# Kernel tuning notes

Hardware: AMD Instinct MI355X
Metric: run time of the kernel (lower is better)

The kernel has to match this reference:

```python
import jax, jax.numpy as jnp
import numpy as np

B, F, L, P, H = 32, 64, 8192, 96, 8
HD = F // H
EPS_ATTN = 1e-6
EPS_REVIN = 1e-5
EPS_LN = 1e-5


def setup_inputs() -> dict:
    key = jax.random.key(0)
    ks = jax.random.split(key, 8)
    f32 = jnp.float32
    return {
        'x': jax.random.normal(ks[0], (B, F, L), dtype=f32),
        'gamma': jnp.ones((1, 1, F), dtype=f32),
        'beta': jnp.zeros((1, 1, F), dtype=f32),
        'ln_w': jnp.ones((F,), dtype=f32),
        'ln_b': jnp.zeros((F,), dtype=f32),
        'Wq': 0.05 * jax.random.normal(ks[1], (F, F), dtype=f32),
        'bq': jnp.zeros((F,), dtype=f32),
        'Wk': 0.05 * jax.random.normal(ks[2], (F, F), dtype=f32),
        'bk': jnp.zeros((F,), dtype=f32),
        'Wv': 0.05 * jax.random.normal(ks[3], (F, F), dtype=f32),
        'bv': jnp.zeros((F,), dtype=f32),
        'Wo': 0.05 * jax.random.normal(ks[4], (F, F), dtype=f32),
        'bo': jnp.zeros((F,), dtype=f32),
        'Wlin': 0.01 * jax.random.normal(ks[5], (P, L), dtype=f32),
        'blin': jnp.zeros((P,), dtype=f32),
        'Wp': 0.1 * jax.random.normal(ks[6], (1, F), dtype=f32),
        'bp': jnp.zeros((1,), dtype=f32),
    }


def _phi(t):
    # feature map: elu(x) + 1 (non-negative)
    return jax.nn.elu(t) + 1.0


def _layernorm(h, w, b):
    mu = jnp.mean(h, axis=-1, keepdims=True)
    var = jnp.mean(jnp.square(h - mu), axis=-1, keepdims=True)
    return (h - mu) * jax.lax.rsqrt(var + EPS_LN) * w + b


def reference(x, gamma, beta, ln_w, ln_b, Wq, bq, Wk, bk, Wv, bv, Wo, bo,
              Wlin, blin, Wp, bp):
    # (B, F, L) -> (B, L, F)
    xt = jnp.transpose(x, (0, 2, 1))
    # RevIN norm (stats over time axis, detached; torch std is unbiased ddof=1)
    mean = jax.lax.stop_gradient(jnp.mean(xt, axis=1, keepdims=True))
    std = jax.lax.stop_gradient(jnp.std(xt, axis=1, keepdims=True, ddof=1) + EPS_REVIN)
    xn = (xt - mean) / std * gamma + beta
    residual = xn
    h = _layernorm(xn, ln_w, ln_b)
    # Q/K/V projections (torch Linear: h @ W.T + b)
    Q = h @ Wq.T + bq
    K = h @ Wk.T + bk
    V = h @ Wv.T + bv
    # (B, L, F) -> (B, H, L, HD)
    def heads(t):
        return jnp.transpose(t.reshape(B, L, H, HD), (0, 2, 1, 3))
    Q, K, V = heads(Q), heads(K), heads(V)
    Q, K = _phi(Q), _phi(K)
    # linear attention: phi(Q) (phi(K)^T V) / (phi(Q) sum_n phi(K))
    KV = jnp.einsum('bhnd,bhne->bhde', K, V)           # (B,H,HD,HD)
    out = jnp.einsum('bhnd,bhde->bhne', Q, KV)          # (B,H,L,HD)
    Z = jnp.sum(K, axis=2)                              # (B,H,HD)
    normalizer = jnp.einsum('bhnd,bhd->bhn', Q, Z)[..., None] + EPS_ATTN
    out = out / normalizer
    out = jnp.transpose(out, (0, 2, 1, 3)).reshape(B, L, F)
    out = out @ Wo.T + bo
    y = out + residual                                  # (B, L, F)
    # temporal linear: (B, F, L) @ Wlin.T -> (B, F, P) -> (B, P, F)
    y = jnp.transpose(jnp.transpose(y, (0, 2, 1)) @ Wlin.T + blin, (0, 2, 1))
    # RevIN denorm
    y = (y - beta) / gamma
    y = y * std + mean
    # projector to scalar per step
    return (y @ Wp.T + bp)[..., 0]                      # (B, P)
```

## Files before the change

kernel.cpp:

```cpp
#include <hip/hip_runtime.h>
#include <cstddef>

#define NB 32
#define NF 64
#define NL 8192
#define NP 96
#define NH 8
#define TSPLIT 32

#define WS_MEAN 0
#define WS_STD  2048
#define WS_RSTD 4096
#define WS_KV   6144
#define WS_Z    22528
#define WS_OUT2 24576
#define WS_WLB  221184
#define WS_YT   614400

typedef __bf16 bfx8 __attribute__((ext_vector_type(8)));
typedef float f32x4 __attribute__((ext_vector_type(4)));
#define MFMA16(a, b, c) __builtin_amdgcn_mfma_f32_16x16x32_bf16((a), (b), (c), 0, 0, 0)

__device__ __forceinline__ unsigned short f2bf(float f) {
  unsigned u = __float_as_uint(f);
  unsigned r = u + 0x7FFFu + ((u >> 16) & 1u);
  return (unsigned short)(r >> 16);
}
__device__ __forceinline__ unsigned packbf2(float lo, float hi) {
  return (unsigned)f2bf(lo) | ((unsigned)f2bf(hi) << 16);
}
__device__ __forceinline__ float bflo(unsigned d) { return __uint_as_float(d << 16); }
__device__ __forceinline__ float bfhi(unsigned d) { return __uint_as_float(d & 0xFFFF0000u); }
__device__ __forceinline__ float bf1(unsigned short s) { return __uint_as_float(((unsigned)s) << 16); }

__device__ __forceinline__ bfx8 ldfrag(const unsigned short* p) {
  uint4 u = *(const uint4*)p;
  return __builtin_bit_cast(bfx8, u);
}

__global__ __launch_bounds__(256) void k_stats(const float* __restrict__ x,
                                               float* __restrict__ wmean,
                                               float* __restrict__ wstd,
                                               float* __restrict__ wrstd) {
  int bf = blockIdx.x;
  int tid = threadIdx.x;
  const float4* row4 = (const float4*)(x + (size_t)bf * NL);
  float s1 = 0.f, s2 = 0.f;
#pragma unroll
  for (int i = 0; i < NL / 4 / 256; i++) {
    float4 v = row4[tid + i * 256];
    s1 += v.x + v.y + v.z + v.w;
    s2 += v.x * v.x + v.y * v.y + v.z * v.z + v.w * v.w;
  }
  __shared__ float r1[256], r2[256];
  r1[tid] = s1; r2[tid] = s2;
  __syncthreads();
  for (int off = 128; off > 0; off >>= 1) {
    if (tid < off) { r1[tid] += r1[tid + off]; r2[tid] += r2[tid + off]; }
    __syncthreads();
  }
  if (tid == 0) {
    float m = r1[0] * (1.f / NL);
    float var = (r2[0] - (float)NL * m * m) * (1.f / (NL - 1));
    float sd = sqrtf(fmaxf(var, 0.f)) + 1e-5f;
    wmean[bf] = m;
    wstd[bf] = sd;
    wrstd[bf] = 1.f / sd;
  }
}

__global__ __launch_bounds__(256) void k_wlb(const float* __restrict__ Wlin,
                                             unsigned short* __restrict__ wlb) {
  int i = blockIdx.x * 256 + threadIdx.x;
  float4 v = ((const float4*)Wlin)[i];
  uint2 o; o.x = packbf2(v.x, v.y); o.y = packbf2(v.z, v.w);
  *(uint2*)&wlb[i * 4] = o;
}

__global__ __launch_bounds__(256, 4) void k_kv(
    const float* __restrict__ x,
    const float* __restrict__ gamma, const float* __restrict__ beta,
    const float* __restrict__ lnw, const float* __restrict__ lnb,
    const float* __restrict__ Wk, const float* __restrict__ bk,
    const float* __restrict__ Wv, const float* __restrict__ bv,
    const float* __restrict__ wmean, const float* __restrict__ wrstd,
    float* __restrict__ wKV, float* __restrict__ wZ) {
  __shared__ __align__(16) char smem[40960];
  unsigned short* hA  = (unsigned short*)smem;
  unsigned short* WkB = (unsigned short*)(smem + 18432);
  unsigned short* WvB = (unsigned short*)(smem + 27648);
  unsigned short* pK  = (unsigned short*)smem;
  unsigned short* pV  = (unsigned short*)(smem + 17408);
  float* SkT   = (float*)(smem + 36864);
  float* Tpart = (float*)(smem + 37888);
  float* mun   = (float*)(smem + 39936);
  float* rsn   = (float*)(smem + 40448);

  const int tid = threadIdx.x;
  const int b = blockIdx.x >> 6;
  const int L0 = (blockIdx.x & 63) * 128;
  const int lane = tid & 63, wv = tid >> 6;
  const int mm = lane & 15, qd = lane >> 4;

  {
    int jj = tid >> 2, g = tid & 3;
    int f0 = g * 16;
    float tkp = 0.f, tvp = 0.f;
#pragma unroll
    for (int i = 0; i < 4; i++) {
      int f = f0 + i * 4;
      float4 wk4 = *(const float4*)&Wk[jj * NF + f];
      float4 wv4 = *(const float4*)&Wv[jj * NF + f];
      float4 lw  = *(const float4*)&lnw[f];
      float4 lb  = *(const float4*)&lnb[f];
      uint2 pk2, pv2;
      pk2.x = packbf2(wk4.x * lw.x, wk4.y * lw.y);
      pk2.y = packbf2(wk4.z * lw.z, wk4.w * lw.w);
      pv2.x = packbf2(wv4.x * lw.x, wv4.y * lw.y);
      pv2.y = packbf2(wv4.z * lw.z, wv4.w * lw.w);
      *(uint2*)&WkB[jj * 72 + f] = pk2;
      *(uint2*)&WvB[jj * 72 + f] = pv2;
      tkp += lb.x * wk4.x + lb.y * wk4.y + lb.z * wk4.z + lb.w * wk4.w;
      tvp += lb.x * wv4.x + lb.y * wv4.y + lb.z * wv4.z + lb.w * wv4.w;
    }
    Tpart[g * 64 + jj] = tkp;
    Tpart[256 + g * 64 + jj] = tvp;
  }

  if (tid < 128) {
    float xn[NF];
    float mu = 0.f;
#pragma unroll
    for (int f = 0; f < NF; f++) {
      float v = x[((size_t)(b * NF + f)) * NL + L0 + tid];
      v = (v - wmean[b * NF + f]) * wrstd[b * NF + f] * gamma[f] + beta[f];
      xn[f] = v; mu += v;
    }
    mu *= (1.f / NF);
    float var = 0.f;
#pragma unroll
    for (int f = 0; f < NF; f++) { float d = xn[f] - mu; var += d * d; }
    float rs = rsqrtf(var * (1.f / NF) + 1e-5f);
    mun[tid] = mu; rsn[tid] = rs;
    unsigned* hrow = (unsigned*)&hA[tid * 72];
#pragma unroll
    for (int f2 = 0; f2 < 32; f2++)
      hrow[f2] = packbf2(xn[2 * f2], xn[2 * f2 + 1]);
  }
  __syncthreads();

  if (tid < 128) {
    int sel = tid >> 6, j = tid & 63;
    const unsigned* wr = (const unsigned*)((sel ? WvB : WkB) + j * 72);
    float s = 0.f;
#pragma unroll
    for (int i = 0; i < 32; i++) { unsigned d = wr[i]; s += bflo(d) + bfhi(d); }
    float t = Tpart[sel * 256 + j] + Tpart[sel * 256 + 64 + j] +
              Tpart[sel * 256 + 128 + j] + Tpart[sel * 256 + 192 + j];
    t += sel ? bv[j] : bk[j];
    SkT[sel * 128 + j] = s;
    SkT[sel * 128 + 64 + j] = t;
  }
  __syncthreads();

  const f32x4 fz = {0.f, 0.f, 0.f, 0.f};
  f32x4 kacc[2][4], vacc[2][4];
#pragma unroll
  for (int i = 0; i < 2; i++)
#pragma unroll
    for (int jt = 0; jt < 4; jt++) { kacc[i][jt] = fz; vacc[i][jt] = fz; }

#pragma unroll
  for (int kc = 0; kc < 2; kc++) {
    bfx8 a0 = ldfrag(&hA[(wv * 32 + mm) * 72 + kc * 32 + qd * 8]);
    bfx8 a1 = ldfrag(&hA[(wv * 32 + 16 + mm) * 72 + kc * 32 + qd * 8]);
#pragma unroll
    for (int jt = 0; jt < 4; jt++) {
      bfx8 bkf = ldfrag(&WkB[(jt * 16 + mm) * 72 + kc * 32 + qd * 8]);
      bfx8 bvf = ldfrag(&WvB[(jt * 16 + mm) * 72 + kc * 32 + qd * 8]);
      kacc[0][jt] = MFMA16(a0, bkf, kacc[0][jt]);
      kacc[1][jt] = MFMA16(a1, bkf, kacc[1][jt]);
      vacc[0][jt] = MFMA16(a0, bvf, vacc[0][jt]);
      vacc[1][jt] = MFMA16(a1, bvf, vacc[1][jt]);
    }
  }

#pragma unroll
  for (int lt2 = 0; lt2 < 2; lt2++) {
    float4 mu4 = *(const float4*)&mun[wv * 32 + lt2 * 16 + qd * 4];
    float4 rs4 = *(const float4*)&rsn[wv * 32 + lt2 * 16 + qd * 4];
    float muv[4] = {mu4.x, mu4.y, mu4.z, mu4.w};
    float rsv[4] = {rs4.x, rs4.y, rs4.z, rs4.w};
#pragma unroll
    for (int jt = 0; jt < 4; jt++) {
      int j = jt * 16 + mm;
      float Sk = SkT[j], Tk = SkT[64 + j], Sv = SkT[128 + j], Tv = SkT[192 + j];
#pragma unroll
      for (int r = 0; r < 4; r++) {
        float kk = rsv[r] * (kacc[lt2][jt][r] - muv[r] * Sk) + Tk;
        kacc[lt2][jt][r] = (kk > 0.f) ? (kk + 1.f) : __expf(kk);
        vacc[lt2][jt][r] = rsv[r] * (vacc[lt2][jt][r] - muv[r] * Sv) + Tv;
      }
    }
  }
  __syncthreads();

#pragma unroll
  for (int lt2 = 0; lt2 < 2; lt2++) {
    int l0 = wv * 32 + lt2 * 16 + qd * 4;
#pragma unroll
    for (int jt = 0; jt < 4; jt++) {
      int j = jt * 16 + mm;
      uint2 dk, dv;
      dk.x = packbf2(kacc[lt2][jt][0], kacc[lt2][jt][1]);
      dk.y = packbf2(kacc[lt2][jt][2], kacc[lt2][jt][3]);
      dv.x = packbf2(vacc[lt2][jt][0], vacc[lt2][jt][1]);
      dv.y = packbf2(vacc[lt2][jt][2], vacc[lt2][jt][3]);
      *(uint2*)&pK[j * 136 + l0] = dk;
      *(uint2*)&pV[j * 136 + l0] = dv;
    }
  }
  __syncthreads();

  {
    f32x4 racc = fz;
#pragma unroll
    for (int kb = 0; kb < 4; kb++) {
      bfx8 ak = ldfrag(&pK[(wv * 16 + mm) * 136 + kb * 32 + qd * 8]);
      bfx8 bv8 = ldfrag(&pV[(wv * 16 + mm) * 136 + kb * 32 + qd * 8]);
      racc = MFMA16(ak, bv8, racc);
    }
    int eh = mm >> 3, e = mm & 7;
#pragma unroll
    for (int r = 0; r < 4; r++) {
      int row = qd * 4 + r;
      if ((row >> 3) == eh)
        atomicAdd(&wKV[(b * NH + wv * 2 + eh) * 64 + (row & 7) * 8 + e], racc[r]);
    }
  }
  if (tid < 64) {
    const unsigned* kr = (const unsigned*)&pK[tid * 136];
    float zs = 0.f;
#pragma unroll
    for (int i = 0; i < 64; i++) { unsigned d = kr[i]; zs += bflo(d) + bfhi(d); }
    atomicAdd(&wZ[b * 64 + tid], zs);
  }
}

__global__ __launch_bounds__(256, 2) void k_qy(
    const float* __restrict__ x,
    const float* __restrict__ gamma, const float* __restrict__ beta,
    const float* __restrict__ lnw, const float* __restrict__ lnb,
    const float* __restrict__ Wq, const float* __restrict__ bq,
    const float* __restrict__ Wo, const float* __restrict__ bo,
    const float* __restrict__ wmean, const float* __restrict__ wrstd,
    const float* __restrict__ wKV, const float* __restrict__ wZ,
    unsigned short* __restrict__ yTb) {
  __shared__ __align__(16) char smem[60160];
  unsigned short* hA  = (unsigned short*)smem;
  unsigned short* WqB = (unsigned short*)(smem + 18432);
  unsigned short* WoB = (unsigned short*)(smem + 27648);
  unsigned short* qaA = (unsigned short*)(smem + 36864);
  float* kvz   = (float*)(smem + 55296);
  float* mun   = (float*)(smem + 57600);
  float* rsn   = (float*)(smem + 58112);
  float* SqTq  = (float*)(smem + 58624);
  float* Tpart = (float*)(smem + 59136);

  const int tid = threadIdx.x;
  const int b = blockIdx.x >> 6;
  const int L0 = (blockIdx.x & 63) * 128;
  const int lane = tid & 63, wv = tid >> 6;
  const int mm = lane & 15, qd = lane >> 4;

  {
    int jj = tid >> 2, g = tid & 3;
    int f0 = g * 16;
    float tqp = 0.f;
#pragma unroll
    for (int i = 0; i < 4; i++) {
      int f = f0 + i * 4;
      float4 wq4 = *(const float4*)&Wq[jj * NF + f];
      float4 wo4 = *(const float4*)&Wo[jj * NF + f];
      float4 lw  = *(const float4*)&lnw[f];
      float4 lb  = *(const float4*)&lnb[f];
      uint2 pq2, po2;
      pq2.x = packbf2(wq4.x * lw.x, wq4.y * lw.y);
      pq2.y = packbf2(wq4.z * lw.z, wq4.w * lw.w);
      po2.x = packbf2(wo4.x, wo4.y);
      po2.y = packbf2(wo4.z, wo4.w);
      *(uint2*)&WqB[jj * 72 + f] = pq2;
      *(uint2*)&WoB[jj * 72 + f] = po2;
      tqp += lb.x * wq4.x + lb.y * wq4.y + lb.z * wq4.z + lb.w * wq4.w;
    }
    Tpart[g * 64 + jj] = tqp;
  }
  for (int i = tid; i < 576; i += 256)
    kvz[i] = (i < 512) ? wKV[b * 512 + i] : wZ[b * 64 + i - 512];

  if (tid < 128) {
    float xn[NF];
    float mu = 0.f;
#pragma unroll
    for (int f = 0; f < NF; f++) {
      float v = x[((size_t)(b * NF + f)) * NL + L0 + tid];
      v = (v - wmean[b * NF + f]) * wrstd[b * NF + f] * gamma[f] + beta[f];
      xn[f] = v; mu += v;
    }
    mu *= (1.f / NF);
    float var = 0.f;
#pragma unroll
    for (int f = 0; f < NF; f++) { float d = xn[f] - mu; var += d * d; }
    float rs = rsqrtf(var * (1.f / NF) + 1e-5f);
    mun[tid] = mu; rsn[tid] = rs;
    unsigned* hrow = (unsigned*)&hA[tid * 72];
#pragma unroll
    for (int f2 = 0; f2 < 32; f2++)
      hrow[f2] = packbf2(xn[2 * f2], xn[2 * f2 + 1]);
  }
  __syncthreads();

  if (tid < 64) {
    const unsigned* wr = (const unsigned*)(WqB + tid * 72);
    float s = 0.f;
#pragma unroll
    for (int i = 0; i < 32; i++) { unsigned d = wr[i]; s += bflo(d) + bfhi(d); }
    float t = Tpart[tid] + Tpart[64 + tid] + Tpart[128 + tid] + Tpart[192 + tid] + bq[tid];
    SqTq[tid] = s; SqTq[64 + tid] = t;
  }
  __syncthreads();

  const f32x4 fz = {0.f, 0.f, 0.f, 0.f};

  {
    f32x4 qacc[2][4];
#pragma unroll
    for (int i = 0; i < 2; i++)
#pragma unroll
      for (int jt = 0; jt < 4; jt++) qacc[i][jt] = fz;
#pragma unroll
    for (int kc = 0; kc < 2; kc++) {
      bfx8 a0 = ldfrag(&hA[(wv * 32 + mm) * 72 + kc * 32 + qd * 8]);
      bfx8 a1 = ldfrag(&hA[(wv * 32 + 16 + mm) * 72 + kc * 32 + qd * 8]);
#pragma unroll
      for (int jt = 0; jt < 4; jt++) {
        bfx8 bqf = ldfrag(&WqB[(jt * 16 + mm) * 72 + kc * 32 + qd * 8]);
        qacc[0][jt] = MFMA16(a0, bqf, qacc[0][jt]);
        qacc[1][jt] = MFMA16(a1, bqf, qacc[1][jt]);
      }
    }
#pragma unroll
    for (int lt2 = 0; lt2 < 2; lt2++) {
      float4 mu4 = *(const float4*)&mun[wv * 32 + lt2 * 16 + qd * 4];
      float4 rs4 = *(const float4*)&rsn[wv * 32 + lt2 * 16 + qd * 4];
      float muv[4] = {mu4.x, mu4.y, mu4.z, mu4.w};
      float rsv[4] = {rs4.x, rs4.y, rs4.z, rs4.w};
      int l0 = wv * 32 + lt2 * 16 + qd * 4;
#pragma unroll
      for (int jt = 0; jt < 4; jt++) {
        int j = jt * 16 + mm;
        float Sj = SqTq[j], Tj = SqTq[64 + j];
#pragma unroll
        for (int r = 0; r < 4; r++) {
          float q = rsv[r] * (qacc[lt2][jt][r] - muv[r] * Sj) + Tj;
          q = (q > 0.f) ? (q + 1.f) : __expf(q);
          qaA[(l0 + r) * 72 + j] = f2bf(q);
        }
      }
    }
  }
  __syncthreads();

  {
    int lt = tid & 31, hd = tid >> 5;
    int lbase = lt * 4;
    float qv[4][8];
#pragma unroll
    for (int i = 0; i < 4; i++) {
      uint4 u = *(const uint4*)&qaA[(lbase + i) * 72 + hd * 8];
      qv[i][0] = bflo(u.x); qv[i][1] = bfhi(u.x);
      qv[i][2] = bflo(u.y); qv[i][3] = bfhi(u.y);
      qv[i][4] = bflo(u.z); qv[i][5] = bfhi(u.z);
      qv[i][6] = bflo(u.w); qv[i][7] = bfhi(u.w);
    }
    float att[4][8], nrm[4];
#pragma unroll
    for (int i = 0; i < 4; i++) {
      nrm[i] = 1e-6f;
#pragma unroll
      for (int e = 0; e < 8; e++) att[i][e] = 0.f;
    }
#pragma unroll
    for (int d = 0; d < 8; d++) {
      float zd = kvz[512 + hd * 8 + d];
      float4 kva = *(const float4*)&kvz[hd * 64 + d * 8];
      float4 kvb = *(const float4*)&kvz[hd * 64 + d * 8 + 4];
#pragma unroll
      for (int i = 0; i < 4; i++) {
        float qq = qv[i][d];
        nrm[i] = fmaf(qq, zd, nrm[i]);
        att[i][0] = fmaf(qq, kva.x, att[i][0]);
        att[i][1] = fmaf(qq, kva.y, att[i][1]);
        att[i][2] = fmaf(qq, kva.z, att[i][2]);
        att[i][3] = fmaf(qq, kva.w, att[i][3]);
        att[i][4] = fmaf(qq, kvb.x, att[i][4]);
        att[i][5] = fmaf(qq, kvb.y, att[i][5]);
        att[i][6] = fmaf(qq, kvb.z, att[i][6]);
        att[i][7] = fmaf(qq, kvb.w, att[i][7]);
      }
    }
#pragma unroll
    for (int i = 0; i < 4; i++) {
      float inv = 1.f / nrm[i];
      uint4 o;
      o.x = packbf2(att[i][0] * inv, att[i][1] * inv);
      o.y = packbf2(att[i][2] * inv, att[i][3] * inv);
      o.z = packbf2(att[i][4] * inv, att[i][5] * inv);
      o.w = packbf2(att[i][6] * inv, att[i][7] * inv);
      *(uint4*)&qaA[(lbase + i) * 72 + hd * 8] = o;
    }
  }
  __syncthreads();

  {
    f32x4 yacc[2][4];
#pragma unroll
    for (int i = 0; i < 2; i++)
#pragma unroll
      for (int ft = 0; ft < 4; ft++) yacc[i][ft] = fz;
#pragma unroll
    for (int ec = 0; ec < 2; ec++) {
      bfx8 a0 = ldfrag(&qaA[(wv * 32 + mm) * 72 + ec * 32 + qd * 8]);
      bfx8 a1 = ldfrag(&qaA[(wv * 32 + 16 + mm) * 72 + ec * 32 + qd * 8]);
#pragma unroll
      for (int ft = 0; ft < 4; ft++) {
        bfx8 bof = ldfrag(&WoB[(ft * 16 + mm) * 72 + ec * 32 + qd * 8]);
        yacc[0][ft] = MFMA16(a0, bof, yacc[0][ft]);
        yacc[1][ft] = MFMA16(a1, bof, yacc[1][ft]);
      }
    }
#pragma unroll
    for (int lt2 = 0; lt2 < 2; lt2++) {
      int l0 = wv * 32 + lt2 * 16 + qd * 4;
#pragma unroll
      for (int ft = 0; ft < 4; ft++) {
        int ff = ft * 16 + mm;
        float bof = bo[ff];
        float v0 = yacc[lt2][ft][0] + bf1(hA[(l0 + 0) * 72 + ff]) + bof;
        float v1 = yacc[lt2][ft][1] + bf1(hA[(l0 + 1) * 72 + ff]) + bof;
        float v2 = yacc[lt2][ft][2] + bf1(hA[(l0 + 2) * 72 + ff]) + bof;
        float v3 = yacc[lt2][ft][3] + bf1(hA[(l0 + 3) * 72 + ff]) + bof;
        uint2 o2;
        o2.x = packbf2(v0, v1);
        o2.y = packbf2(v2, v3);
        *(uint2*)&yTb[((size_t)(b * NF + ff)) * NL + L0 + l0] = o2;
      }
    }
  }
}

__global__ __launch_bounds__(256) void k_temporal(
    const unsigned short* __restrict__ yTb, const unsigned short* __restrict__ wlb,
    float* __restrict__ out2) {
  const int tid = threadIdx.x, lane = tid & 63, wvx = tid >> 6;
  const int mm = lane & 15, qd = lane >> 4;
  const int b = blockIdx.x / TSPLIT;
  const int kc = blockIdx.x % TSPLIT;
  const int Lc = NL / TSPLIT;
  const unsigned short* yrow = yTb + ((size_t)(b * NF + wvx * 16 + mm)) * NL + kc * Lc + qd * 8;
  const unsigned short* wrow = wlb + (size_t)mm * NL + kc * Lc + qd * 8;
  const f32x4 fz = {0.f, 0.f, 0.f, 0.f};
  f32x4 acc[6];
#pragma unroll
  for (int pt = 0; pt < 6; pt++) acc[pt] = fz;

#pragma unroll 2
  for (int ks = 0; ks < Lc / 32; ks++) {
    bfx8 bfr = ldfrag(yrow + ks * 32);
#pragma unroll
    for (int pt = 0; pt < 6; pt++) {
      bfx8 afr = ldfrag(wrow + (size_t)(pt * 16) * NL + ks * 32);
      acc[pt] = MFMA16(afr, bfr, acc[pt]);
    }
  }
  const int ff = wvx * 16 + mm;
#pragma unroll
  for (int pt = 0; pt < 6; pt++) {
#pragma unroll
    for (int r = 0; r < 4; r++) {
      int p = pt * 16 + qd * 4 + r;
      atomicAdd(&out2[((size_t)(b * NP + p)) * NF + ff], acc[pt][r]);
    }
  }
}

__global__ __launch_bounds__(64) void k_final(
    const float* __restrict__ out2, const float* __restrict__ blin,
    const float* __restrict__ gamma, const float* __restrict__ beta,
    const float* __restrict__ wmean, const float* __restrict__ wstd,
    const float* __restrict__ Wp, const float* __restrict__ bp,
    float* __restrict__ out) {
  int b = blockIdx.x / NP;
  int p = blockIdx.x % NP;
  int f = threadIdx.x;
  float v = out2[((size_t)(b * NP + p)) * NF + f] + blin[p];
  v = (v - beta[f]) / gamma[f];
  v = v * wstd[b * NF + f] + wmean[b * NF + f];
  float s = v * Wp[f];
#pragma unroll
  for (int off = 32; off > 0; off >>= 1)
    s += __shfl_down(s, off, 64);
  if (f == 0) out[blockIdx.x] = s + bp[0];
}

extern "C" void kernel_launch(void* const* d_in, const int* in_sizes, int n_in,
                              void* d_out, int out_size, void* d_ws, size_t ws_size,
                              hipStream_t stream) {
  const float* x     = (const float*)d_in[0];
  const float* gamma = (const float*)d_in[1];
  const float* beta  = (const float*)d_in[2];
  const float* lnw   = (const float*)d_in[3];
  const float* lnb   = (const float*)d_in[4];
  const float* Wq    = (const float*)d_in[5];
  const float* bq    = (const float*)d_in[6];
  const float* Wk    = (const float*)d_in[7];
  const float* bk    = (const float*)d_in[8];
  const float* Wv    = (const float*)d_in[9];
  const float* bv    = (const float*)d_in[10];
  const float* Wo    = (const float*)d_in[11];
  const float* bo    = (const float*)d_in[12];
  const float* Wlin  = (const float*)d_in[13];
  const float* blin  = (const float*)d_in[14];
  const float* Wp    = (const float*)d_in[15];
  const float* bp    = (const float*)d_in[16];
  float* out = (float*)d_out;
  float* ws  = (float*)d_ws;

  float* wmean = ws + WS_MEAN;
  float* wstd  = ws + WS_STD;
  float* wrstd = ws + WS_RSTD;
  float* wKV   = ws + WS_KV;
  float* wZ    = ws + WS_Z;
  float* wout2 = ws + WS_OUT2;
  unsigned short* wlb = (unsigned short*)(ws + WS_WLB);
  unsigned short* yTb = (unsigned short*)(ws + WS_YT);

  (void)hipMemsetAsync(wKV, 0, (size_t)(16384 + 2048 + 196608) * sizeof(float), stream);

  k_stats<<<NB * NF, 256, 0, stream>>>(x, wmean, wstd, wrstd);
  k_wlb<<<NP * NL / 4 / 256, 256, 0, stream>>>(Wlin, wlb);
  k_kv<<<NB * 64, 256, 0, stream>>>(x, gamma, beta, lnw, lnb, Wk, bk, Wv, bv,
                                    wmean, wrstd, wKV, wZ);
  k_qy<<<NB * 64, 256, 0, stream>>>(x, gamma, beta, lnw, lnb, Wq, bq, Wo, bo,
                                    wmean, wrstd, wKV, wZ, yTb);
  k_temporal<<<NB * TSPLIT, 256, 0, stream>>>(yTb, wlb, wout2);
  k_final<<<NB * NP, 64, 0, stream>>>(wout2, blin, gamma, beta, wmean, wstd, Wp, bp, out);
}
```

Baseline: 247.1 us.

## Cache normalized bf16 activations from k_kv and retile yT/Wlin for contiguous MFMA loads

k_kv now writes its bf16 normalized tile and per-row LayerNorm stats to workspace, so k_qy no longer rereads fp32 x and redoes RevIN/LayerNorm. k_qy drops to a smaller LDS footprint, which lets it raise occupancy to 3 blocks per CU, and it reads the residual from the global bf16 tile. The yT and Wlin bf16 buffers are re-laid out in 32-wide L blocks so k_temporal's fragment loads are contiguous. The cost is extra global writes and reads (a 16 MB bf16 intermediate) and a larger workspace.

```diff
diff --git a/kernel.cpp b/kernel.cpp
--- a/kernel.cpp
+++ b/kernel.cpp
@@ -14,8 +14,11 @@
 #define WS_KV   6144
 #define WS_Z    22528
 #define WS_OUT2 24576
-#define WS_WLB  221184
-#define WS_YT   614400
+#define WS_MUN  221184
+#define WS_RSN  483328
+#define WS_WLB  745472
+#define WS_XNB  1138688
+#define WS_YT   9527296
 
 typedef __bf16 bfx8 __attribute__((ext_vector_type(8)));
 typedef float f32x4 __attribute__((ext_vector_type(4)));
@@ -72,9 +75,14 @@
 __global__ __launch_bounds__(256) void k_wlb(const float* __restrict__ Wlin,
                                              unsigned short* __restrict__ wlb) {
   int i = blockIdx.x * 256 + threadIdx.x;
-  float4 v = ((const float4*)Wlin)[i];
-  uint2 o; o.x = packbf2(v.x, v.y); o.y = packbf2(v.z, v.w);
-  *(uint2*)&wlb[i * 4] = o;
+  int p = i >> 10;
+  int l8 = (i & 1023) * 8;
+  float4 va = *(const float4*)&Wlin[(size_t)p * NL + l8];
+  float4 vb = *(const float4*)&Wlin[(size_t)p * NL + l8 + 4];
+  uint4 o;
+  o.x = packbf2(va.x, va.y); o.y = packbf2(va.z, va.w);
+  o.z = packbf2(vb.x, vb.y); o.w = packbf2(vb.z, vb.w);
+  *(uint4*)&wlb[(((size_t)(l8 >> 5)) * NP + p) * 32 + (l8 & 31)] = o;
 }
 
 __global__ __launch_bounds__(256, 4) void k_kv(
@@ -84,7 +92,9 @@
     const float* __restrict__ Wk, const float* __restrict__ bk,
     const float* __restrict__ Wv, const float* __restrict__ bv,
     const float* __restrict__ wmean, const float* __restrict__ wrstd,
-    float* __restrict__ wKV, float* __restrict__ wZ) {
+    float* __restrict__ wKV, float* __restrict__ wZ,
+    float* __restrict__ wmun, float* __restrict__ wrsn,
+    unsigned short* __restrict__ xnb) {
   __shared__ __align__(16) char smem[40960];
   unsigned short* hA  = (unsigned short*)smem;
   unsigned short* WkB = (unsigned short*)(smem + 18432);
@@ -98,7 +108,8 @@
 
   const int tid = threadIdx.x;
   const int b = blockIdx.x >> 6;
-  const int L0 = (blockIdx.x & 63) * 128;
+  const int tI = blockIdx.x & 63;
+  const int L0 = tI * 128;
   const int lane = tid & 63, wv = tid >> 6;
   const int mm = lane & 15, qd = lane >> 4;
 
@@ -142,12 +153,21 @@
     for (int f = 0; f < NF; f++) { float d = xn[f] - mu; var += d * d; }
     float rs = rsqrtf(var * (1.f / NF) + 1e-5f);
     mun[tid] = mu; rsn[tid] = rs;
+    wmun[(size_t)b * NL + L0 + tid] = mu;
+    wrsn[(size_t)b * NL + L0 + tid] = rs;
     unsigned* hrow = (unsigned*)&hA[tid * 72];
 #pragma unroll
     for (int f2 = 0; f2 < 32; f2++)
       hrow[f2] = packbf2(xn[2 * f2], xn[2 * f2 + 1]);
   }
   __syncthreads();
+
+  {
+    int row = tid >> 1, half = tid & 1;
+    const uint4* s4 = (const uint4*)&hA[row * 72 + half * 32];
+    uint4* d4 = (uint4*)(xnb + (((size_t)(b * 64 + tI) * 128 + row) * 64 + half * 32));
+    d4[0] = s4[0]; d4[1] = s4[1]; d4[2] = s4[2]; d4[3] = s4[3];
+  }
 
   if (tid < 128) {
     int sel = tid >> 6, j = tid & 63;
@@ -247,31 +267,32 @@
   }
 }
 
-__global__ __launch_bounds__(256, 2) void k_qy(
-    const float* __restrict__ x,
-    const float* __restrict__ gamma, const float* __restrict__ beta,
+__global__ __launch_bounds__(256, 3) void k_qy(
+    const unsigned short* __restrict__ xnb,
     const float* __restrict__ lnw, const float* __restrict__ lnb,
     const float* __restrict__ Wq, const float* __restrict__ bq,
     const float* __restrict__ Wo, const float* __restrict__ bo,
-    const float* __restrict__ wmean, const float* __restrict__ wrstd,
+    const float* __restrict__ wmun, const float* __restrict__ wrsn,
     const float* __restrict__ wKV, const float* __restrict__ wZ,
-    unsigned short* __restrict__ yTb) {
-  __shared__ __align__(16) char smem[60160];
+    unsigned short* __restrict__ ytb) {
+  __shared__ __align__(16) char smem[41728];
   unsigned short* hA  = (unsigned short*)smem;
+  unsigned short* qaA = (unsigned short*)smem;
   unsigned short* WqB = (unsigned short*)(smem + 18432);
   unsigned short* WoB = (unsigned short*)(smem + 27648);
-  unsigned short* qaA = (unsigned short*)(smem + 36864);
-  float* kvz   = (float*)(smem + 55296);
-  float* mun   = (float*)(smem + 57600);
-  float* rsn   = (float*)(smem + 58112);
-  float* SqTq  = (float*)(smem + 58624);
-  float* Tpart = (float*)(smem + 59136);
+  float* kvz   = (float*)(smem + 36864);
+  float* mun   = (float*)(smem + 39168);
+  float* rsn   = (float*)(smem + 39680);
+  float* SqTq  = (float*)(smem + 40192);
+  float* Tpart = (float*)(smem + 40704);
 
   const int tid = threadIdx.x;
   const int b = blockIdx.x >> 6;
-  const int L0 = (blockIdx.x & 63) * 128;
+  const int tI = blockIdx.x & 63;
+  const int L0 = tI * 128;
   const int lane = tid & 63, wv = tid >> 6;
   const int mm = lane & 15, qd = lane >> 4;
+  const unsigned short* xtile = xnb + (size_t)(b * 64 + tI) * 128 * 64;
 
   {
     int jj = tid >> 2, g = tid & 3;
@@ -297,26 +318,16 @@
   }
   for (int i = tid; i < 576; i += 256)
     kvz[i] = (i < 512) ? wKV[b * 512 + i] : wZ[b * 64 + i - 512];
-
+  {
+    int row = tid >> 1, half = tid & 1;
+    const uint4* s4 = (const uint4*)(xtile + (size_t)row * 64 + half * 32);
+    uint4 u0 = s4[0], u1 = s4[1], u2 = s4[2], u3 = s4[3];
+    uint4* d4 = (uint4*)&hA[row * 72 + half * 32];
+    d4[0] = u0; d4[1] = u1; d4[2] = u2; d4[3] = u3;
+  }
   if (tid < 128) {
-    float xn[NF];
-    float mu = 0.f;
-#pragma unroll
-    for (int f = 0; f < NF; f++) {
-      float v = x[((size_t)(b * NF + f)) * NL + L0 + tid];
-      v = (v - wmean[b * NF + f]) * wrstd[b * NF + f] * gamma[f] + beta[f];
-      xn[f] = v; mu += v;
-    }
-    mu *= (1.f / NF);
-    float var = 0.f;
-#pragma unroll
-    for (int f = 0; f < NF; f++) { float d = xn[f] - mu; var += d * d; }
-    float rs = rsqrtf(var * (1.f / NF) + 1e-5f);
-    mun[tid] = mu; rsn[tid] = rs;
-    unsigned* hrow = (unsigned*)&hA[tid * 72];
-#pragma unroll
-    for (int f2 = 0; f2 < 32; f2++)
-      hrow[f2] = packbf2(xn[2 * f2], xn[2 * f2 + 1]);
+    mun[tid] = wmun[(size_t)b * NL + L0 + tid];
+    rsn[tid] = wrsn[(size_t)b * NL + L0 + tid];
   }
   __syncthreads();
 
@@ -446,40 +457,39 @@
       for (int ft = 0; ft < 4; ft++) {
         int ff = ft * 16 + mm;
         float bof = bo[ff];
-        float v0 = yacc[lt2][ft][0] + bf1(hA[(l0 + 0) * 72 + ff]) + bof;
-        float v1 = yacc[lt2][ft][1] + bf1(hA[(l0 + 1) * 72 + ff]) + bof;
-        float v2 = yacc[lt2][ft][2] + bf1(hA[(l0 + 2) * 72 + ff]) + bof;
-        float v3 = yacc[lt2][ft][3] + bf1(hA[(l0 + 3) * 72 + ff]) + bof;
+        float v0 = yacc[lt2][ft][0] + bf1(xtile[(size_t)(l0 + 0) * 64 + ff]) + bof;
+        float v1 = yacc[lt2][ft][1] + bf1(xtile[(size_t)(l0 + 1) * 64 + ff]) + bof;
+        float v2 = yacc[lt2][ft][2] + bf1(xtile[(size_t)(l0 + 2) * 64 + ff]) + bof;
+        float v3 = yacc[lt2][ft][3] + bf1(xtile[(size_t)(l0 + 3) * 64 + ff]) + bof;
         uint2 o2;
         o2.x = packbf2(v0, v1);
         o2.y = packbf2(v2, v3);
-        *(uint2*)&yTb[((size_t)(b * NF + ff)) * NL + L0 + l0] = o2;
+        size_t idx = (((size_t)b * (NL / 32) + (L0 >> 5) + wv) * 64 + ff) * 32 + lt2 * 16 + qd * 4;
+        *(uint2*)&ytb[idx] = o2;
       }
     }
   }
 }
 
 __global__ __launch_bounds__(256) void k_temporal(
-    const unsigned short* __restrict__ yTb, const unsigned short* __restrict__ wlb,
+    const unsigned short* __restrict__ ytb, const unsigned short* __restrict__ wlb,
     float* __restrict__ out2) {
   const int tid = threadIdx.x, lane = tid & 63, wvx = tid >> 6;
   const int mm = lane & 15, qd = lane >> 4;
   const int b = blockIdx.x / TSPLIT;
   const int kc = blockIdx.x % TSPLIT;
-  const int Lc = NL / TSPLIT;
-  const unsigned short* yrow = yTb + ((size_t)(b * NF + wvx * 16 + mm)) * NL + kc * Lc + qd * 8;
-  const unsigned short* wrow = wlb + (size_t)mm * NL + kc * Lc + qd * 8;
   const f32x4 fz = {0.f, 0.f, 0.f, 0.f};
   f32x4 acc[6];
 #pragma unroll
   for (int pt = 0; pt < 6; pt++) acc[pt] = fz;
 
 #pragma unroll 2
-  for (int ks = 0; ks < Lc / 32; ks++) {
-    bfx8 bfr = ldfrag(yrow + ks * 32);
+  for (int ks = 0; ks < 8; ks++) {
+    int lg = kc * 8 + ks;
+    bfx8 bfr = ldfrag(&ytb[(((size_t)b * (NL / 32) + lg) * 64 + wvx * 16 + mm) * 32 + qd * 8]);
 #pragma unroll
     for (int pt = 0; pt < 6; pt++) {
-      bfx8 afr = ldfrag(wrow + (size_t)(pt * 16) * NL + ks * 32);
+      bfx8 afr = ldfrag(&wlb[((size_t)lg * NP + pt * 16 + mm) * 32 + qd * 8]);
       acc[pt] = MFMA16(afr, bfr, acc[pt]);
     }
   }
@@ -542,17 +552,20 @@
   float* wKV   = ws + WS_KV;
   float* wZ    = ws + WS_Z;
   float* wout2 = ws + WS_OUT2;
+  float* wmun  = ws + WS_MUN;
+  float* wrsn  = ws + WS_RSN;
   unsigned short* wlb = (unsigned short*)(ws + WS_WLB);
-  unsigned short* yTb = (unsigned short*)(ws + WS_YT);
+  unsigned short* xnb = (unsigned short*)(ws + WS_XNB);
+  unsigned short* ytb = (unsigned short*)(ws + WS_YT);
 
   (void)hipMemsetAsync(wKV, 0, (size_t)(16384 + 2048 + 196608) * sizeof(float), stream);
 
   k_stats<<<NB * NF, 256, 0, stream>>>(x, wmean, wstd, wrstd);
-  k_wlb<<<NP * NL / 4 / 256, 256, 0, stream>>>(Wlin, wlb);
+  k_wlb<<<NP * NL / 8 / 256, 256, 0, stream>>>(Wlin, wlb);
   k_kv<<<NB * 64, 256, 0, stream>>>(x, gamma, beta, lnw, lnb, Wk, bk, Wv, bv,
-                                    wmean, wrstd, wKV, wZ);
-  k_qy<<<NB * 64, 256, 0, stream>>>(x, gamma, beta, lnw, lnb, Wq, bq, Wo, bo,
-                                    wmean, wrstd, wKV, wZ, yTb);
-  k_temporal<<<NB * TSPLIT, 256, 0, stream>>>(yTb, wlb, wout2);
+                                    wmean, wrstd, wKV, wZ, wmun, wrsn, xnb);
+  k_qy<<<NB * 64, 256, 0, stream>>>(xnb, lnw, lnb, Wq, bq, Wo, bo,
+                                    wmun, wrsn, wKV, wZ, ytb);
+  k_temporal<<<NB * TSPLIT, 256, 0, stream>>>(ytb, wlb, wout2);
   k_final<<<NB * NP, 64, 0, stream>>>(wout2, blin, gamma, beta, wmean, wstd, Wp, bp, out);
 }
```

Result: faster. 233.9 us (-5.3%).
